# Kernel tuning notes

Hardware: AMD Instinct MI355X
Metric: run time of the kernel (lower is better)

Reference implementation:

```python
import jax, jax.numpy as jnp
import numpy as np

N_GROUP, D, DFF = 8, 256, 1024
T = 131072  # total routed tokens


def setup_inputs() -> dict:
    key = jax.random.key(0)
    k_x, k_g, k_u, k_d = jax.random.split(key, 4)
    # kaiming_uniform_(a=sqrt(5)) over fan_in == second-to-last dim
    def kaiming(k, shape, fan_in):
        bound = 1.0 / np.sqrt(fan_in)
        return jax.random.uniform(k, shape, jnp.float32, -bound, bound)
    x = jax.random.normal(k_x, (T, D), jnp.float32)
    weight_gate = kaiming(k_g, (N_GROUP, D, DFF), D)
    weight_up = kaiming(k_u, (N_GROUP, D, DFF), D)
    weight_down = kaiming(k_d, (N_GROUP, DFF, D), DFF)
    # cumulative group end offsets; uniform groups of T // N_GROUP tokens
    offs = (jnp.arange(1, N_GROUP + 1, dtype=jnp.int32) * (T // N_GROUP))
    return {"x": x, "weight_gate": weight_gate, "weight_up": weight_up,
            "weight_down": weight_down, "offs": offs}


def reference(x, weight_gate, weight_up, weight_down, offs):
    # Grouped GLU: for tokens in group g, y = silu(x @ Wg_gate) * (x @ Wg_up) @ Wg_down.
    # offs encodes uniform group boundaries (offs[i] = (i+1)*T/G), so the grouped
    # GEMM is a batched matmul over the expert axis after a reshape.
    G = weight_gate.shape[0]
    t, d = x.shape
    xg = x.reshape(G, t // G, d)                                  # [G, Tg, d]
    z_gate = jnp.einsum('gtd,gdf->gtf', xg, weight_gate)          # [G, Tg, dff]
    z_up = jnp.einsum('gtd,gdf->gtf', xg, weight_up)
    h = jax.nn.silu(z_gate) * z_up
    y = jnp.einsum('gtf,gfd->gtd', h, weight_down)                # [G, Tg, d]
    return y.reshape(t, d)
```

## Files before the change

### kernel.cpp

```cpp
#include <hip/hip_runtime.h>

typedef __bf16 bf16x8 __attribute__((ext_vector_type(8)));
typedef float f32x16 __attribute__((ext_vector_type(16)));
typedef unsigned int u32x4 __attribute__((ext_vector_type(4)));

#define NGROUP 8
#define DMODEL 256
#define DFF    1024
#define TTOT   131072
#define TGRP   (TTOT / NGROUP)
#define MTILE  256
#define NCHUNK 32

__device__ __forceinline__ unsigned int f2bf(float f) {
    unsigned int x = __builtin_bit_cast(unsigned int, f);
    return (x + 0x7fffu + ((x >> 16) & 1u)) >> 16;
}
__device__ __forceinline__ unsigned int pack2(float lo, float hi) {
    return f2bf(lo) | (f2bf(hi) << 16);
}
__device__ __forceinline__ unsigned int cvtpk(float lo, float hi) {
    unsigned int r;
    asm("v_cvt_pk_bf16_f32 %0, %1, %2" : "=v"(r) : "v"(lo), "v"(hi));
    return r;
}

__device__ __forceinline__ void g2l(const void* g, void* l) {
    __builtin_amdgcn_global_load_lds(
        (const __attribute__((address_space(1))) unsigned int*)g,
        (__attribute__((address_space(3))) unsigned int*)l, 16, 0, 0);
}

__global__ void k_prep_w(const float* __restrict__ wg, const float* __restrict__ wu,
                         const float* __restrict__ wd, u32x4* __restrict__ out) {
    int t = blockIdx.x * 256 + threadIdx.x;
    int lane = t & 63;
    int q = lane >> 5, l31 = lane & 31;
    int fg = t >> 6;
    int fid = fg % 48;
    int gc  = fg / 48;
    int c = gc & 31, g = gc >> 5;
    u32x4 v;
    if (fid < 32) {
        const float* w = (fid < 16) ? wg : wu;
        int ks = fid & 15;
        const float* src = w + (size_t)(g * 256 + ks * 16 + q * 8) * 1024 + c * 32 + l31;
        v = u32x4{ pack2(src[0],        src[1024]),
                   pack2(src[2 * 1024], src[3 * 1024]),
                   pack2(src[4 * 1024], src[5 * 1024]),
                   pack2(src[6 * 1024], src[7 * 1024]) };
    } else {
        int idx = fid - 32;
        int ks2 = idx >> 3, nb = idx & 7;
        const float* src = wd + (size_t)(g * 1024 + c * 32 + ks2 * 16 + q * 4) * 256 + nb * 32 + l31;
        v = u32x4{ pack2(src[0 * 256],  src[1 * 256]),
                   pack2(src[2 * 256],  src[3 * 256]),
                   pack2(src[8 * 256],  src[9 * 256]),
                   pack2(src[10 * 256], src[11 * 256]) };
    }
    out[t] = v;
}

__global__ __launch_bounds__(512, 2)
void k_glu(const float* __restrict__ x,
           const u32x4* __restrict__ wcomb,
           float* __restrict__ y) {
    __shared__ u32x4 smem[6144];

    const int tid  = threadIdx.x;
    const int lane = tid & 63;
    const int w    = tid >> 6;
    const int q    = lane >> 5;
    const int l31  = lane & 31;

    const int g    = blockIdx.x & 7;
    const int m0   = g * TGRP + (blockIdx.x >> 3) * MTILE;
    const int tok  = m0 + w * 32 + l31;

    const u32x4* wcg = wcomb + (size_t)(g * 32) * 3072;

    {
        #pragma unroll
        for (int i = 0; i < 6; ++i) {
            int off = i * 512 + w * 64;
            g2l(wcg + off + lane, smem + off);
        }
    }
    u32x4 xf[16];
    {
        const float* xrow = x + (size_t)tok * DMODEL + q * 8;
        #pragma unroll
        for (int ks = 0; ks < 16; ++ks) {
            float4 a = *(const float4*)(xrow + ks * 16);
            float4 b = *(const float4*)(xrow + ks * 16 + 4);
            xf[ks] = u32x4{ cvtpk(a.x, a.y), cvtpk(a.z, a.w),
                            cvtpk(b.x, b.y), cvtpk(b.z, b.w) };
        }
    }

    f32x16 acc[8];
    #pragma unroll
    for (int nb = 0; nb < 8; ++nb)
        #pragma unroll
        for (int i = 0; i < 16; ++i) acc[nb][i] = 0.0f;

    asm volatile("s_waitcnt vmcnt(0)" ::: "memory");
    __builtin_amdgcn_s_barrier();
    asm volatile("" ::: "memory");

    for (int c = 0; c < NCHUNK; ++c) {
        const u32x4* sb = smem + (c & 1) * 3072;

        if (c + 1 < NCHUNK) {
            u32x4* db = smem + ((c + 1) & 1) * 3072;
            const u32x4* gsrc = wcg + (size_t)(c + 1) * 3072;
            #pragma unroll
            for (int i = 0; i < 6; ++i) {
                int off = i * 512 + w * 64;
                g2l(gsrc + off + lane, db + off);
            }
            asm volatile("s_waitcnt vmcnt(6)" ::: "memory");
        } else {
            asm volatile("s_waitcnt vmcnt(0)" ::: "memory");
        }
        __builtin_amdgcn_s_barrier();
        asm volatile("" ::: "memory");

        f32x16 zg, zu;
        #pragma unroll
        for (int i = 0; i < 16; ++i) { zg[i] = 0.0f; zu[i] = 0.0f; }
        __builtin_amdgcn_s_setprio(1);
        #pragma unroll
        for (int ks = 0; ks < 16; ++ks) {
            const u32x4 a1 = sb[ks * 64 + lane];
            const u32x4 a2 = sb[1024 + ks * 64 + lane];
            zg = __builtin_amdgcn_mfma_f32_32x32x16_bf16(
                     __builtin_bit_cast(bf16x8, a1),
                     __builtin_bit_cast(bf16x8, xf[ks]), zg, 0, 0, 0);
            zu = __builtin_amdgcn_mfma_f32_32x32x16_bf16(
                     __builtin_bit_cast(bf16x8, a2),
                     __builtin_bit_cast(bf16x8, xf[ks]), zu, 0, 0, 0);
        }
        __builtin_amdgcn_s_setprio(0);

        float hv[16];
        #pragma unroll
        for (int i = 0; i < 16; ++i) {
            const float gv = zg[i];
            const float s  = __builtin_amdgcn_rcpf(1.0f + __expf(-gv));
            hv[i] = gv * s * zu[i];
        }
        const u32x4 ha0 = u32x4{ cvtpk(hv[0], hv[1]),   cvtpk(hv[2], hv[3]),
                                 cvtpk(hv[4], hv[5]),   cvtpk(hv[6], hv[7]) };
        const u32x4 ha1 = u32x4{ cvtpk(hv[8], hv[9]),   cvtpk(hv[10], hv[11]),
                                 cvtpk(hv[12], hv[13]), cvtpk(hv[14], hv[15]) };
        const bf16x8 A0 = __builtin_bit_cast(bf16x8, ha0);
        const bf16x8 A1 = __builtin_bit_cast(bf16x8, ha1);

        __builtin_amdgcn_s_setprio(1);
        #pragma unroll
        for (int nb = 0; nb < 8; ++nb) {
            acc[nb] = __builtin_amdgcn_mfma_f32_32x32x16_bf16(
                          A0, __builtin_bit_cast(bf16x8, sb[2048 + nb * 64 + lane]),
                          acc[nb], 0, 0, 0);
        }
        #pragma unroll
        for (int nb = 0; nb < 8; ++nb) {
            acc[nb] = __builtin_amdgcn_mfma_f32_32x32x16_bf16(
                          A1, __builtin_bit_cast(bf16x8, sb[2048 + (8 + nb) * 64 + lane]),
                          acc[nb], 0, 0, 0);
        }
        __builtin_amdgcn_s_setprio(0);

        asm volatile("" ::: "memory");
        __builtin_amdgcn_s_barrier();
    }

    float* yp = y + (size_t)(m0 + w * 32) * DMODEL;
    #pragma unroll
    for (int nb = 0; nb < 8; ++nb) {
        const int col = nb * 32 + l31;
        #pragma unroll
        for (int r = 0; r < 16; ++r) {
            const int row = (r & 3) + (r >> 2) * 8 + q * 4;
            yp[(size_t)row * DMODEL + col] = acc[nb][r];
        }
    }
}

extern "C" void kernel_launch(void* const* d_in, const int* in_sizes, int n_in,
                              void* d_out, int out_size, void* d_ws, size_t ws_size,
                              hipStream_t stream) {
    const float* x  = (const float*)d_in[0];
    const float* wg = (const float*)d_in[1];
    const float* wu = (const float*)d_in[2];
    const float* wd = (const float*)d_in[3];
    float* y = (float*)d_out;

    u32x4* wcomb = (u32x4*)d_ws;

    k_prep_w<<<dim3(3072), dim3(256), 0, stream>>>(wg, wu, wd, wcomb);
    k_glu<<<dim3(512), dim3(512), 0, stream>>>(x, wcomb, y);
}
```

Measured before the change: 414.5 us.

## Stream down-proj weights from global into registers and triple-buffer gate/up in LDS

LDS now holds only the gate/up weight fragments of each chunk. They are triple-buffered and prefetched two chunks ahead, so each chunk needs one barrier instead of two. Down-projection weights are read straight from global memory into registers with inline-asm loads, staged in groups of four with explicit vmcnt waits that interleave them with the MFMAs. This aims to cut LDS traffic and barrier cost. In exchange, all eight waves fetch the same down weights separately, which raises L2 traffic and register pressure. The trailing vmcnt(0) also waits on the prefetch each iteration, which can shorten the effective prefetch distance.

```diff
diff --git a/kernel.cpp b/kernel.cpp
--- a/kernel.cpp
+++ b/kernel.cpp
@@ -29,6 +29,12 @@
     __builtin_amdgcn_global_load_lds(
         (const __attribute__((address_space(1))) unsigned int*)g,
         (__attribute__((address_space(3))) unsigned int*)l, 16, 0, 0);
+}
+
+__device__ __forceinline__ u32x4 gld16(const u32x4* p) {
+    u32x4 d;
+    asm volatile("global_load_dwordx4 %0, %1, off" : "=v"(d) : "v"(p) : "memory");
+    return d;
 }
 
 __global__ void k_prep_w(const float* __restrict__ wg, const float* __restrict__ wu,
@@ -79,12 +85,15 @@
 
     const u32x4* wcg = wcomb + (size_t)(g * 32) * 3072;
 
-    {
-        #pragma unroll
-        for (int i = 0; i < 6; ++i) {
-            int off = i * 512 + w * 64;
-            g2l(wcg + off + lane, smem + off);
-        }
+    #pragma unroll
+    for (int i = 0; i < 4; ++i) {
+        int off = i * 512 + w * 64;
+        g2l(wcg + off + lane, smem + off);
+    }
+    #pragma unroll
+    for (int i = 0; i < 4; ++i) {
+        int off = i * 512 + w * 64;
+        g2l(wcg + 3072 + off + lane, smem + 2048 + off);
     }
     u32x4 xf[16];
     {
@@ -105,26 +114,24 @@
         for (int i = 0; i < 16; ++i) acc[nb][i] = 0.0f;
 
     asm volatile("s_waitcnt vmcnt(0)" ::: "memory");
-    __builtin_amdgcn_s_barrier();
-    asm volatile("" ::: "memory");
-
+
+    int bcur = 0;
     for (int c = 0; c < NCHUNK; ++c) {
-        const u32x4* sb = smem + (c & 1) * 3072;
-
-        if (c + 1 < NCHUNK) {
-            u32x4* db = smem + ((c + 1) & 1) * 3072;
-            const u32x4* gsrc = wcg + (size_t)(c + 1) * 3072;
+        __builtin_amdgcn_s_barrier();
+        asm volatile("" ::: "memory");
+
+        if (c < NCHUNK - 2) {
+            const int bst = (bcur == 0) ? 2 : bcur - 1;
+            u32x4* db = smem + bst * 2048;
+            const u32x4* gsrc = wcg + (size_t)(c + 2) * 3072;
             #pragma unroll
-            for (int i = 0; i < 6; ++i) {
+            for (int i = 0; i < 4; ++i) {
                 int off = i * 512 + w * 64;
                 g2l(gsrc + off + lane, db + off);
             }
-            asm volatile("s_waitcnt vmcnt(6)" ::: "memory");
-        } else {
-            asm volatile("s_waitcnt vmcnt(0)" ::: "memory");
-        }
-        __builtin_amdgcn_s_barrier();
-        asm volatile("" ::: "memory");
+        }
+
+        const u32x4* sb = smem + bcur * 2048;
 
         f32x16 zg, zu;
         #pragma unroll
@@ -157,23 +164,55 @@
         const bf16x8 A0 = __builtin_bit_cast(bf16x8, ha0);
         const bf16x8 A1 = __builtin_bit_cast(bf16x8, ha1);
 
-        __builtin_amdgcn_s_setprio(1);
-        #pragma unroll
-        for (int nb = 0; nb < 8; ++nb) {
-            acc[nb] = __builtin_amdgcn_mfma_f32_32x32x16_bf16(
-                          A0, __builtin_bit_cast(bf16x8, sb[2048 + nb * 64 + lane]),
-                          acc[nb], 0, 0, 0);
-        }
-        #pragma unroll
-        for (int nb = 0; nb < 8; ++nb) {
-            acc[nb] = __builtin_amdgcn_mfma_f32_32x32x16_bf16(
-                          A1, __builtin_bit_cast(bf16x8, sb[2048 + (8 + nb) * 64 + lane]),
-                          acc[nb], 0, 0, 0);
-        }
-        __builtin_amdgcn_s_setprio(0);
-
-        asm volatile("" ::: "memory");
-        __builtin_amdgcn_s_barrier();
+        {
+            const u32x4* wdc = wcg + (size_t)c * 3072 + 2048 + lane;
+            u32x4 wa0 = gld16(wdc + 0 * 64), wa1 = gld16(wdc + 1 * 64),
+                  wa2 = gld16(wdc + 2 * 64), wa3 = gld16(wdc + 3 * 64);
+            u32x4 wb0 = gld16(wdc + 4 * 64), wb1 = gld16(wdc + 5 * 64),
+                  wb2 = gld16(wdc + 6 * 64), wb3 = gld16(wdc + 7 * 64);
+
+            asm volatile("s_waitcnt vmcnt(4)" ::: "memory");
+            __builtin_amdgcn_sched_barrier(0);
+            __builtin_amdgcn_s_setprio(1);
+            acc[0] = __builtin_amdgcn_mfma_f32_32x32x16_bf16(A0, __builtin_bit_cast(bf16x8, wa0), acc[0], 0, 0, 0);
+            acc[1] = __builtin_amdgcn_mfma_f32_32x32x16_bf16(A0, __builtin_bit_cast(bf16x8, wa1), acc[1], 0, 0, 0);
+            acc[2] = __builtin_amdgcn_mfma_f32_32x32x16_bf16(A0, __builtin_bit_cast(bf16x8, wa2), acc[2], 0, 0, 0);
+            acc[3] = __builtin_amdgcn_mfma_f32_32x32x16_bf16(A0, __builtin_bit_cast(bf16x8, wa3), acc[3], 0, 0, 0);
+            __builtin_amdgcn_s_setprio(0);
+
+            wa0 = gld16(wdc + 8 * 64);  wa1 = gld16(wdc + 9 * 64);
+            wa2 = gld16(wdc + 10 * 64); wa3 = gld16(wdc + 11 * 64);
+            asm volatile("s_waitcnt vmcnt(4)" ::: "memory");
+            __builtin_amdgcn_sched_barrier(0);
+            __builtin_amdgcn_s_setprio(1);
+            acc[4] = __builtin_amdgcn_mfma_f32_32x32x16_bf16(A0, __builtin_bit_cast(bf16x8, wb0), acc[4], 0, 0, 0);
+            acc[5] = __builtin_amdgcn_mfma_f32_32x32x16_bf16(A0, __builtin_bit_cast(bf16x8, wb1), acc[5], 0, 0, 0);
+            acc[6] = __builtin_amdgcn_mfma_f32_32x32x16_bf16(A0, __builtin_bit_cast(bf16x8, wb2), acc[6], 0, 0, 0);
+            acc[7] = __builtin_amdgcn_mfma_f32_32x32x16_bf16(A0, __builtin_bit_cast(bf16x8, wb3), acc[7], 0, 0, 0);
+            __builtin_amdgcn_s_setprio(0);
+
+            wb0 = gld16(wdc + 12 * 64); wb1 = gld16(wdc + 13 * 64);
+            wb2 = gld16(wdc + 14 * 64); wb3 = gld16(wdc + 15 * 64);
+            asm volatile("s_waitcnt vmcnt(4)" ::: "memory");
+            __builtin_amdgcn_sched_barrier(0);
+            __builtin_amdgcn_s_setprio(1);
+            acc[0] = __builtin_amdgcn_mfma_f32_32x32x16_bf16(A1, __builtin_bit_cast(bf16x8, wa0), acc[0], 0, 0, 0);
+            acc[1] = __builtin_amdgcn_mfma_f32_32x32x16_bf16(A1, __builtin_bit_cast(bf16x8, wa1), acc[1], 0, 0, 0);
+            acc[2] = __builtin_amdgcn_mfma_f32_32x32x16_bf16(A1, __builtin_bit_cast(bf16x8, wa2), acc[2], 0, 0, 0);
+            acc[3] = __builtin_amdgcn_mfma_f32_32x32x16_bf16(A1, __builtin_bit_cast(bf16x8, wa3), acc[3], 0, 0, 0);
+            __builtin_amdgcn_s_setprio(0);
+
+            asm volatile("s_waitcnt vmcnt(0)" ::: "memory");
+            __builtin_amdgcn_sched_barrier(0);
+            __builtin_amdgcn_s_setprio(1);
+            acc[4] = __builtin_amdgcn_mfma_f32_32x32x16_bf16(A1, __builtin_bit_cast(bf16x8, wb0), acc[4], 0, 0, 0);
+            acc[5] = __builtin_amdgcn_mfma_f32_32x32x16_bf16(A1, __builtin_bit_cast(bf16x8, wb1), acc[5], 0, 0, 0);
+            acc[6] = __builtin_amdgcn_mfma_f32_32x32x16_bf16(A1, __builtin_bit_cast(bf16x8, wb2), acc[6], 0, 0, 0);
+            acc[7] = __builtin_amdgcn_mfma_f32_32x32x16_bf16(A1, __builtin_bit_cast(bf16x8, wb3), acc[7], 0, 0, 0);
+            __builtin_amdgcn_s_setprio(0);
+        }
+
+        bcur = (bcur == 2) ? 0 : bcur + 1;
     }
 
     float* yp = y + (size_t)(m0 + w * 32) * DMODEL;
```

New measurement: 429.8 us. 1.04x slower.

## Software-pipeline GLU chunks: overlap down-proj of previous chunk with gate/up of next

Applied to the files above, without the earlier changes.

Restructures the chunk loop into a prologue, steady state and epilogue so that the down-projection MFMAs for chunk c-1 are interleaved with the gate/up MFMAs for chunk c. The SiLU and bf16 packing of one chunk can then overlap with matrix-core work instead of stalling it. LDS goes from double to triple buffering (144 KB), and each iteration now uses one barrier with a full vmcnt(0) wait instead of two barriers. The s_setprio hints are dropped. The larger LDS footprint may limit occupancy to one block per CU, and the full wait may expose load latency.

```diff
diff --git a/kernel.cpp b/kernel.cpp
--- a/kernel.cpp
+++ b/kernel.cpp
@@ -61,11 +61,14 @@
     out[t] = v;
 }
 
+#define MFMA(A, B, C) __builtin_amdgcn_mfma_f32_32x32x16_bf16( \
+        __builtin_bit_cast(bf16x8, A), __builtin_bit_cast(bf16x8, B), C, 0, 0, 0)
+
 __global__ __launch_bounds__(512, 2)
 void k_glu(const float* __restrict__ x,
            const u32x4* __restrict__ wcomb,
            float* __restrict__ y) {
-    __shared__ u32x4 smem[6144];
+    __shared__ u32x4 smem[9216];
 
     const int tid  = threadIdx.x;
     const int lane = tid & 63;
@@ -79,12 +82,15 @@
 
     const u32x4* wcg = wcomb + (size_t)(g * 32) * 3072;
 
-    {
-        #pragma unroll
-        for (int i = 0; i < 6; ++i) {
-            int off = i * 512 + w * 64;
-            g2l(wcg + off + lane, smem + off);
-        }
+    #pragma unroll
+    for (int i = 0; i < 6; ++i) {
+        int off = i * 512 + w * 64;
+        g2l(wcg + off + lane, smem + off);
+    }
+    #pragma unroll
+    for (int i = 0; i < 6; ++i) {
+        int off = i * 512 + w * 64;
+        g2l(wcg + 3072 + off + lane, smem + 3072 + off);
     }
     u32x4 xf[16];
     {
@@ -108,40 +114,65 @@
     __builtin_amdgcn_s_barrier();
     asm volatile("" ::: "memory");
 
-    for (int c = 0; c < NCHUNK; ++c) {
-        const u32x4* sb = smem + (c & 1) * 3072;
+    u32x4 A0, A1;
+
+    {
+        const u32x4* sb = smem;
+        f32x16 zg, zu;
+        #pragma unroll
+        for (int i = 0; i < 16; ++i) { zg[i] = 0.0f; zu[i] = 0.0f; }
+        #pragma unroll
+        for (int ks = 0; ks < 16; ++ks) {
+            const u32x4 a1 = sb[ks * 64 + lane];
+            const u32x4 a2 = sb[1024 + ks * 64 + lane];
+            zg = MFMA(a1, xf[ks], zg);
+            zu = MFMA(a2, xf[ks], zu);
+        }
+        float hv[16];
+        #pragma unroll
+        for (int i = 0; i < 16; ++i) {
+            const float gv = zg[i];
+            const float s  = __builtin_amdgcn_rcpf(1.0f + __expf(-gv));
+            hv[i] = gv * s * zu[i];
+        }
+        A0 = u32x4{ cvtpk(hv[0], hv[1]),   cvtpk(hv[2], hv[3]),
+                    cvtpk(hv[4], hv[5]),   cvtpk(hv[6], hv[7]) };
+        A1 = u32x4{ cvtpk(hv[8], hv[9]),   cvtpk(hv[10], hv[11]),
+                    cvtpk(hv[12], hv[13]), cvtpk(hv[14], hv[15]) };
+    }
+
+    int bc = 1, bp = 0, bn = 2;
+    for (int c = 1; c < NCHUNK; ++c) {
+        const u32x4* sbc = smem + bc * 3072;
+        const u32x4* sbp = smem + bp * 3072;
+
+        asm volatile("s_waitcnt vmcnt(0)" ::: "memory");
+        __builtin_amdgcn_s_barrier();
+        asm volatile("" ::: "memory");
 
         if (c + 1 < NCHUNK) {
-            u32x4* db = smem + ((c + 1) & 1) * 3072;
+            u32x4* db = smem + bn * 3072;
             const u32x4* gsrc = wcg + (size_t)(c + 1) * 3072;
             #pragma unroll
             for (int i = 0; i < 6; ++i) {
                 int off = i * 512 + w * 64;
                 g2l(gsrc + off + lane, db + off);
             }
-            asm volatile("s_waitcnt vmcnt(6)" ::: "memory");
-        } else {
-            asm volatile("s_waitcnt vmcnt(0)" ::: "memory");
-        }
-        __builtin_amdgcn_s_barrier();
-        asm volatile("" ::: "memory");
+        }
 
         f32x16 zg, zu;
         #pragma unroll
         for (int i = 0; i < 16; ++i) { zg[i] = 0.0f; zu[i] = 0.0f; }
-        __builtin_amdgcn_s_setprio(1);
-        #pragma unroll
-        for (int ks = 0; ks < 16; ++ks) {
-            const u32x4 a1 = sb[ks * 64 + lane];
-            const u32x4 a2 = sb[1024 + ks * 64 + lane];
-            zg = __builtin_amdgcn_mfma_f32_32x32x16_bf16(
-                     __builtin_bit_cast(bf16x8, a1),
-                     __builtin_bit_cast(bf16x8, xf[ks]), zg, 0, 0, 0);
-            zu = __builtin_amdgcn_mfma_f32_32x32x16_bf16(
-                     __builtin_bit_cast(bf16x8, a2),
-                     __builtin_bit_cast(bf16x8, xf[ks]), zu, 0, 0, 0);
-        }
-        __builtin_amdgcn_s_setprio(0);
+        #pragma unroll
+        for (int ks = 0; ks < 16; ++ks) {
+            const u32x4 a1 = sbc[ks * 64 + lane];
+            const u32x4 a2 = sbc[1024 + ks * 64 + lane];
+            const u32x4 bd = sbp[2048 + ks * 64 + lane];
+            zg = MFMA(a1, xf[ks], zg);
+            zu = MFMA(a2, xf[ks], zu);
+            if (ks < 8) acc[ks]     = MFMA(A0, bd, acc[ks]);
+            else        acc[ks - 8] = MFMA(A1, bd, acc[ks - 8]);
+        }
 
         float hv[16];
         #pragma unroll
@@ -150,30 +181,22 @@
             const float s  = __builtin_amdgcn_rcpf(1.0f + __expf(-gv));
             hv[i] = gv * s * zu[i];
         }
-        const u32x4 ha0 = u32x4{ cvtpk(hv[0], hv[1]),   cvtpk(hv[2], hv[3]),
-                                 cvtpk(hv[4], hv[5]),   cvtpk(hv[6], hv[7]) };
-        const u32x4 ha1 = u32x4{ cvtpk(hv[8], hv[9]),   cvtpk(hv[10], hv[11]),
-                                 cvtpk(hv[12], hv[13]), cvtpk(hv[14], hv[15]) };
-        const bf16x8 A0 = __builtin_bit_cast(bf16x8, ha0);
-        const bf16x8 A1 = __builtin_bit_cast(bf16x8, ha1);
-
-        __builtin_amdgcn_s_setprio(1);
-        #pragma unroll
-        for (int nb = 0; nb < 8; ++nb) {
-            acc[nb] = __builtin_amdgcn_mfma_f32_32x32x16_bf16(
-                          A0, __builtin_bit_cast(bf16x8, sb[2048 + nb * 64 + lane]),
-                          acc[nb], 0, 0, 0);
-        }
-        #pragma unroll
-        for (int nb = 0; nb < 8; ++nb) {
-            acc[nb] = __builtin_amdgcn_mfma_f32_32x32x16_bf16(
-                          A1, __builtin_bit_cast(bf16x8, sb[2048 + (8 + nb) * 64 + lane]),
-                          acc[nb], 0, 0, 0);
-        }
-        __builtin_amdgcn_s_setprio(0);
-
-        asm volatile("" ::: "memory");
-        __builtin_amdgcn_s_barrier();
+        A0 = u32x4{ cvtpk(hv[0], hv[1]),   cvtpk(hv[2], hv[3]),
+                    cvtpk(hv[4], hv[5]),   cvtpk(hv[6], hv[7]) };
+        A1 = u32x4{ cvtpk(hv[8], hv[9]),   cvtpk(hv[10], hv[11]),
+                    cvtpk(hv[12], hv[13]), cvtpk(hv[14], hv[15]) };
+
+        const int t = bp; bp = bc; bc = bn; bn = t;
+    }
+
+    {
+        const u32x4* sbp = smem + bp * 3072;
+        #pragma unroll
+        for (int ks = 0; ks < 16; ++ks) {
+            const u32x4 bd = sbp[2048 + ks * 64 + lane];
+            if (ks < 8) acc[ks]     = MFMA(A0, bd, acc[ks]);
+            else        acc[ks - 8] = MFMA(A1, bd, acc[ks - 8]);
+        }
     }
 
     float* yp = y + (size_t)(m0 + w * 32) * DMODEL;
```

New measurement: 414.9 us. No clear change (+0.1%).

## Software-pipeline LDS weight reads and drop the trailing per-chunk barrier

Applied to the files above, without the earlier changes.

The compiler-generated LDS loads in both MFMA loops are replaced with inline-asm ds_read_b128 issued one step ahead into double-buffered registers. Explicit lgkmcnt waits and sched_barriers pin the order of loads and MFMAs so LDS latency can overlap with matrix work. The chunk loop is also reorganised to wait and barrier once at the top instead of twice per chunk, relying on the double-buffered shared memory for safety. In exchange, the scheduler loses freedom, the code assumes the shared array sits at LDS address 0, and the global prefetch now has less slack before its vmcnt(0) wait.

```diff
diff --git a/kernel.cpp b/kernel.cpp
--- a/kernel.cpp
+++ b/kernel.cpp
@@ -30,6 +30,17 @@
         (const __attribute__((address_space(1))) unsigned int*)g,
         (__attribute__((address_space(3))) unsigned int*)l, 16, 0, 0);
 }
+
+__device__ __forceinline__ u32x4 dsr(unsigned addr) {
+    u32x4 d;
+    asm volatile("ds_read_b128 %0, %1" : "=v"(d) : "v"(addr));
+    return d;
+}
+#define WAITLGKM(n) asm volatile("s_waitcnt lgkmcnt(" #n ")")
+#define SBAR0()     __builtin_amdgcn_sched_barrier(0)
+
+#define MFMA(A, B, C) __builtin_amdgcn_mfma_f32_32x32x16_bf16( \
+        __builtin_bit_cast(bf16x8, A), __builtin_bit_cast(bf16x8, B), C, 0, 0, 0)
 
 __global__ void k_prep_w(const float* __restrict__ wg, const float* __restrict__ wu,
                          const float* __restrict__ wd, u32x4* __restrict__ out) {
@@ -78,13 +89,12 @@
     const int tok  = m0 + w * 32 + l31;
 
     const u32x4* wcg = wcomb + (size_t)(g * 32) * 3072;
-
-    {
-        #pragma unroll
-        for (int i = 0; i < 6; ++i) {
-            int off = i * 512 + w * 64;
-            g2l(wcg + off + lane, smem + off);
-        }
+    const unsigned lbase = (unsigned)lane * 16u;
+
+    #pragma unroll
+    for (int i = 0; i < 6; ++i) {
+        int off = i * 512 + w * 64;
+        g2l(wcg + off + lane, smem + off);
     }
     u32x4 xf[16];
     {
@@ -104,12 +114,10 @@
         #pragma unroll
         for (int i = 0; i < 16; ++i) acc[nb][i] = 0.0f;
 
-    asm volatile("s_waitcnt vmcnt(0)" ::: "memory");
-    __builtin_amdgcn_s_barrier();
-    asm volatile("" ::: "memory");
-
     for (int c = 0; c < NCHUNK; ++c) {
-        const u32x4* sb = smem + (c & 1) * 3072;
+        asm volatile("s_waitcnt vmcnt(0)" ::: "memory");
+        __builtin_amdgcn_s_barrier();
+        asm volatile("" ::: "memory");
 
         if (c + 1 < NCHUNK) {
             u32x4* db = smem + ((c + 1) & 1) * 3072;
@@ -119,27 +127,29 @@
                 int off = i * 512 + w * 64;
                 g2l(gsrc + off + lane, db + off);
             }
-            asm volatile("s_waitcnt vmcnt(6)" ::: "memory");
-        } else {
-            asm volatile("s_waitcnt vmcnt(0)" ::: "memory");
-        }
-        __builtin_amdgcn_s_barrier();
-        asm volatile("" ::: "memory");
+        }
+
+        const unsigned bb = (unsigned)((c & 1) * 49152) + lbase;
 
         f32x16 zg, zu;
         #pragma unroll
         for (int i = 0; i < 16; ++i) { zg[i] = 0.0f; zu[i] = 0.0f; }
+        u32x4 pa[2], pb[2];
+        pa[0] = dsr(bb);
+        pb[0] = dsr(bb + 16384u);
         __builtin_amdgcn_s_setprio(1);
         #pragma unroll
         for (int ks = 0; ks < 16; ++ks) {
-            const u32x4 a1 = sb[ks * 64 + lane];
-            const u32x4 a2 = sb[1024 + ks * 64 + lane];
-            zg = __builtin_amdgcn_mfma_f32_32x32x16_bf16(
-                     __builtin_bit_cast(bf16x8, a1),
-                     __builtin_bit_cast(bf16x8, xf[ks]), zg, 0, 0, 0);
-            zu = __builtin_amdgcn_mfma_f32_32x32x16_bf16(
-                     __builtin_bit_cast(bf16x8, a2),
-                     __builtin_bit_cast(bf16x8, xf[ks]), zu, 0, 0, 0);
+            if (ks < 15) {
+                pa[(ks + 1) & 1] = dsr(bb + (unsigned)(ks + 1) * 1024u);
+                pb[(ks + 1) & 1] = dsr(bb + 16384u + (unsigned)(ks + 1) * 1024u);
+                WAITLGKM(2);
+            } else {
+                WAITLGKM(0);
+            }
+            SBAR0();
+            zg = MFMA(pa[ks & 1], xf[ks], zg);
+            zu = MFMA(pb[ks & 1], xf[ks], zu);
         }
         __builtin_amdgcn_s_setprio(0);
 
@@ -150,30 +160,27 @@
             const float s  = __builtin_amdgcn_rcpf(1.0f + __expf(-gv));
             hv[i] = gv * s * zu[i];
         }
-        const u32x4 ha0 = u32x4{ cvtpk(hv[0], hv[1]),   cvtpk(hv[2], hv[3]),
-                                 cvtpk(hv[4], hv[5]),   cvtpk(hv[6], hv[7]) };
-        const u32x4 ha1 = u32x4{ cvtpk(hv[8], hv[9]),   cvtpk(hv[10], hv[11]),
-                                 cvtpk(hv[12], hv[13]), cvtpk(hv[14], hv[15]) };
-        const bf16x8 A0 = __builtin_bit_cast(bf16x8, ha0);
-        const bf16x8 A1 = __builtin_bit_cast(bf16x8, ha1);
-
+        const u32x4 A0 = u32x4{ cvtpk(hv[0], hv[1]),   cvtpk(hv[2], hv[3]),
+                                cvtpk(hv[4], hv[5]),   cvtpk(hv[6], hv[7]) };
+        const u32x4 A1 = u32x4{ cvtpk(hv[8], hv[9]),   cvtpk(hv[10], hv[11]),
+                                cvtpk(hv[12], hv[13]), cvtpk(hv[14], hv[15]) };
+
+        u32x4 pd[2];
+        pd[0] = dsr(bb + 32768u);
         __builtin_amdgcn_s_setprio(1);
         #pragma unroll
-        for (int nb = 0; nb < 8; ++nb) {
-            acc[nb] = __builtin_amdgcn_mfma_f32_32x32x16_bf16(
-                          A0, __builtin_bit_cast(bf16x8, sb[2048 + nb * 64 + lane]),
-                          acc[nb], 0, 0, 0);
-        }
-        #pragma unroll
-        for (int nb = 0; nb < 8; ++nb) {
-            acc[nb] = __builtin_amdgcn_mfma_f32_32x32x16_bf16(
-                          A1, __builtin_bit_cast(bf16x8, sb[2048 + (8 + nb) * 64 + lane]),
-                          acc[nb], 0, 0, 0);
+        for (int fi = 0; fi < 16; ++fi) {
+            if (fi < 15) {
+                pd[(fi + 1) & 1] = dsr(bb + 32768u + (unsigned)(fi + 1) * 1024u);
+                WAITLGKM(1);
+            } else {
+                WAITLGKM(0);
+            }
+            SBAR0();
+            if (fi < 8) acc[fi]     = MFMA(A0, pd[fi & 1], acc[fi]);
+            else        acc[fi - 8] = MFMA(A1, pd[fi & 1], acc[fi - 8]);
         }
         __builtin_amdgcn_s_setprio(0);
-
-        asm volatile("" ::: "memory");
-        __builtin_amdgcn_s_barrier();
     }
 
     float* yp = y + (size_t)(m0 + w * 32) * DMODEL;
```

Result: no change. 409.1 us (-1.3%).
